# Optimization experiments

Measured on AMD Instinct MI355X. Metric: run time of the kernel, lower is better.

The kernel has to match this reference:

```python
import jax, jax.numpy as jnp
import numpy as np

S = 4  # MC samples


def _gat_layer(x, mask, w, a_src, a_dst, bias):
    # x: (b,n,fin)  w: (H,fin,fout)  mask: (b,n,n) bool
    h = jnp.einsum('bnf,hfo->bhno', x, w)                      # (b,H,n,fout)
    th = jnp.tanh(h)
    att_src = jnp.einsum('bhno,ho->bhn', th, a_src)
    att_dst = jnp.einsum('bhno,ho->bhn', th, a_dst)
    logits = jax.nn.leaky_relu(att_src[:, :, :, None] + att_dst[:, :, None, :], 0.2)
    logits = jnp.where(mask[:, None, :, :], logits, jnp.float32(-1e9))
    att = jax.nn.softmax(logits, axis=-1)                      # (b,H,n,n)
    out = jnp.einsum('bhij,bhjo->bhio', att, h) + bias         # (b,H,n,fout)
    return out, att


def setup_inputs() -> dict:
    key = jax.random.key(0)
    ks = jax.random.split(key, 11)
    b, n, f0, emb_d = 128, 128, 64, 64
    H1, f1, H2, f2 = 8, 16, 1, 2
    fin1 = f0 + emb_d            # 128 (n_units[0] += 64)
    fin2 = H1 * f1               # 128 (heads concatenated between layers)
    x = jax.random.normal(ks[0], (b, n, f0), jnp.float32)
    emb = jax.random.normal(ks[1], (b, n, emb_d), jnp.float32)
    adj = jax.random.randint(ks[2], (b, n, n), 0, 2).astype(jnp.int32)
    adj = jnp.maximum(adj, jnp.eye(n, dtype=jnp.int32)[None])  # self-loops keep softmax rows valid
    w1 = jax.random.normal(ks[3], (S, H1, fin1, f1), jnp.float32) * 0.1
    a_src1 = jax.random.normal(ks[4], (S, H1, f1), jnp.float32) * 0.1
    a_dst1 = jax.random.normal(ks[5], (S, H1, f1), jnp.float32) * 0.1
    b1 = jax.random.normal(ks[6], (f1,), jnp.float32) * 0.1
    w2 = jax.random.normal(ks[7], (S, H2, fin2, f2), jnp.float32) * 0.1
    a_src2 = jax.random.normal(ks[8], (S, H2, f2), jnp.float32) * 0.1
    a_dst2 = jax.random.normal(ks[9], (S, H2, f2), jnp.float32) * 0.1
    b2 = jax.random.normal(ks[10], (f2,), jnp.float32) * 0.1
    return dict(x=x, emb=emb, adj=adj, w1=w1, a_src1=a_src1, a_dst1=a_dst1, b1=b1,
                w2=w2, a_src2=a_src2, a_dst2=a_dst2, b2=b2)


def reference(x, emb, adj, w1, a_src1, a_dst1, b1, w2, a_src2, a_dst2, b2):
    mask = adj.astype(bool)
    x0 = jnp.concatenate([x, emb], axis=-1)                    # (b,n,128)
    b, n = x0.shape[0], x0.shape[1]
    xs = jnp.broadcast_to(x0, (S,) + x0.shape)                 # same input for each MC sample
    layer = jax.vmap(_gat_layer, in_axes=(0, None, 0, 0, 0, None))
    # layer 1 (per-sample variational weights), ELU activation
    h1, att1 = layer(xs, mask, w1, a_src1, a_dst1, b1)         # h1: (S,b,H1,n,f1)
    h1 = jax.nn.elu(h1)
    # concat heads: transpose(1,2).view(bs,n,-1)
    xs2 = jnp.transpose(h1, (0, 1, 3, 2, 4)).reshape(S, b, n, -1)
    # layer 2 (last layer): no activation, mean over heads
    h2, att2 = layer(xs2, mask, w2, a_src2, a_dst2, b2)        # (S,b,1,n,2)
    out = h2.mean(axis=2)                                      # (S,b,n,2)
    logp = jax.nn.log_softmax(out, axis=-1)[:, :, -1, :]       # (S,b,2) -> ego node
    result = jnp.mean(logp, axis=0)                            # var_mean -> mean (return_uncertainty=False)
    return result
```

## Files before the change

kernel.cpp:

```cpp
#include <hip/hip_runtime.h>
#include <stdint.h>
#include <math.h>

typedef __attribute__((ext_vector_type(8))) short short8;
typedef __attribute__((ext_vector_type(4))) float floatx4;

#define L_HF    0
#define L_SRC   16384
#define L_DST   18432
#define L_MASK  20480
#define L_H2P   22528
#define L_SIZE  26624

union F8 { short8 s8; uint32_t u[4]; };

#if __has_builtin(__builtin_amdgcn_exp2f)
#define EXP2F __builtin_amdgcn_exp2f
#else
#define EXP2F exp2f
#endif
#define LOG2E 1.4426950408889634f

__device__ __forceinline__ uint32_t packbf(float a, float b){
  uint32_t ua = __float_as_uint(a), ub = __float_as_uint(b);
  uint32_t ra = (ua + 0x7fffu + ((ua>>16)&1u)) >> 16;
  uint32_t rb = (ub + 0x7fffu + ((ub>>16)&1u)) >> 16;
  return ra | (rb<<16);
}
__device__ __forceinline__ uint32_t packbf_t(float a, float b){
  return __builtin_amdgcn_perm(__float_as_uint(b), __float_as_uint(a), 0x07060302u);
}
__device__ __forceinline__ float fast_tanh(float x){
  float e = __expf(2.f*x);
  return 1.f - 2.f*__builtin_amdgcn_rcpf(e + 1.f);
}

__global__ __launch_bounds__(512,8) void gat_fused(
    const float* __restrict__ x,  const float* __restrict__ emb,
    const int* __restrict__ adj,  const float* __restrict__ w1,
    const float* __restrict__ a_src1, const float* __restrict__ a_dst1,
    const float* __restrict__ b1, const float* __restrict__ w2,
    float* __restrict__ ws_h2)
{
  __shared__ __align__(16) char smem[L_SIZE];
  char*     hf    = smem + L_HF;
  uint32_t* hf_u  = (uint32_t*)(smem + L_HF);
  float*    src_l = (float*)(smem + L_SRC);
  float*    dst_l = (float*)(smem + L_DST);
  uint32_t* mask_l= (uint32_t*)(smem + L_MASK);
  const uint4* mask4 = (const uint4*)(smem + L_MASK);
  float2*   h2p   = (float2*)(smem + L_H2P);

  const int t    = threadIdx.x;
  const int blk  = blockIdx.x;
  const int s    = blk >> 8;
  const int bb   = (blk & 255) >> 1;
  const int half = blk & 1;
  const int lane = t & 63, w = t >> 6;
  const int of = lane & 15, kg = lane >> 4;

  const int arow = w*16 + of;
  const float* xrow = x   + ((size_t)bb*128 + arow)*64;
  const float* erow = emb + ((size_t)bb*128 + arow)*64;
  short8 af[4];
  #pragma unroll
  for (int ks=0; ks<4; ++ks){
    int k = ks*32 + kg*8;
    const float* p = (k<64) ? (xrow+k) : (erow + (k-64));
    float4 f0 = *(const float4*)p, f1 = *(const float4*)(p+4);
    F8 fr;
    fr.u[0]=packbf(f0.x,f0.y); fr.u[1]=packbf(f0.z,f0.w);
    fr.u[2]=packbf(f1.x,f1.y); fr.u[3]=packbf(f1.z,f1.w);
    af[ks]=fr.s8;
  }

  {
    const float* w1s = w1 + (size_t)s*16384 + half*8192;
    #pragma unroll
    for (int r=0; r<2; ++r){
      int q = t + r*512;
      int ql = q & 63, ks = (q>>6)&3, ct = q>>8;
      const float* wp = w1s + ct*2048 + (ks*32 + (ql>>4)*8)*16 + (ql&15);
      F8 fr;
      fr.u[0]=packbf(wp[0],  wp[16]);
      fr.u[1]=packbf(wp[32], wp[48]);
      fr.u[2]=packbf(wp[64], wp[80]);
      fr.u[3]=packbf(wp[96], wp[112]);
      *(short8*)(hf + ((ct*4+ks)*64 + ql)*16) = fr.s8;
    }
  }

  {
    const int* adjb = adj + (size_t)bb*16384;
    #pragma unroll 4
    for (int rr=0; rr<16; ++rr){
      const int row = w*16 + rr;
      const int* ar = adjb + row*128;
      uint64_t m0 = __ballot(ar[lane] != 0);
      uint64_t m1 = __ballot(ar[64+lane] != 0);
      if (lane == 0)
        ((uint4*)mask_l)[row] = make_uint4((uint32_t)m0,(uint32_t)(m0>>32),
                                           (uint32_t)m1,(uint32_t)(m1>>32));
    }
  }
  __syncthreads();

  floatx4 acc[4];
  #pragma unroll
  for (int ct=0; ct<4; ++ct) acc[ct]=(floatx4){0.f,0.f,0.f,0.f};
  #pragma unroll
  for (int ct=0; ct<4; ++ct)
    #pragma unroll
    for (int ks=0; ks<4; ++ks){
      short8 bfr = *(const short8*)(hf + ((ct*4+ks)*64 + lane)*16);
      acc[ct] = __builtin_amdgcn_mfma_f32_16x16x32_bf16(af[ks], bfr, acc[ct], 0,0,0);
    }
  __syncthreads();

  const int ks_h = w>>1, kgp = (w&1)*2 + (kg>>1), vv = (kg&1)*2;
  #pragma unroll
  for (int ct=0; ct<4; ++ct){
    const int ghd = half*4 + ct;
    float asv = a_src1[s*128 + ghd*16 + of] * LOG2E;
    float adv = a_dst1[s*128 + ghd*16 + of] * LOG2E;
    float ps[4], pd[4];
    #pragma unroll
    for (int r=0; r<4; ++r){
      float th = fast_tanh(acc[ct][r]);
      ps[r] = th*asv; pd[r] = th*adv;
    }
    #pragma unroll
    for (int off=1; off<16; off<<=1)
      #pragma unroll
      for (int r=0; r<4; ++r){ ps[r]+=__shfl_xor(ps[r],off); pd[r]+=__shfl_xor(pd[r],off); }
    if (of==0){
      #pragma unroll
      for (int r=0; r<4; ++r){
        int i = w*16 + kg*4 + r;
        src_l[ct*128+i]=ps[r]; dst_l[ct*128+i]=pd[r];
      }
    }
    uint32_t p0 = packbf(acc[ct][0], acc[ct][1]);
    uint32_t p1 = packbf(acc[ct][2], acc[ct][3]);
    uint32_t* dsth = hf_u + ((ct*4+ks_h)*64 + kgp*16 + of)*4 + vv;
    *(uint2*)dsth = make_uint2(p0, p1);
  }
  __syncthreads();

  const int lhd = w >> 1;
  const int ghd = half*4 + lhd;
  float b1v  = b1[of];
  float w2c0 = w2[s*256 + (ghd*16+of)*2 + 0];
  float w2c1 = w2[s*256 + (ghd*16+of)*2 + 1];
  short8 hb[4];
  #pragma unroll
  for (int ks=0; ks<4; ++ks)
    hb[ks] = *(const short8*)(hf + ((lhd*4+ks)*64 + lane)*16);

  #pragma unroll
  for (int rtl=0; rtl<4; ++rtl){
    const int rt = (w&1)*4 + rtl;
    const int im = rt*16 + of;
    float srcv = src_l[lhd*128 + im];
    uint4 mrow = mask4[im];
    floatx4 acc2 = (floatx4){0.f,0.f,0.f,0.f};
    float zp = 0.f;
    #pragma unroll
    for (int ks=0; ks<4; ++ks){
      const float* dp = dst_l + lhd*128 + ks*32 + kg*8;
      float4 d0 = *(const float4*)dp, d1 = *(const float4*)(dp+4);
      uint32_t mw = (ks==0)?mrow.x:(ks==1)?mrow.y:(ks==2)?mrow.z:mrow.w;
      uint32_t mbyte = mw >> (kg*8);
      float dj[8] = {d0.x,d0.y,d0.z,d0.w,d1.x,d1.y,d1.z,d1.w};
      float e[8];
      #pragma unroll
      for (int jj=0; jj<8; ++jj){
        float t0 = srcv + dj[jj];
        float lr = fmaxf(t0, 0.2f*t0);
        float ev = EXP2F(lr);
        ev = ((mbyte>>jj)&1u) ? ev : 0.f;
        e[jj]=ev; zp += ev;
      }
      F8 fr;
      fr.u[0]=packbf_t(e[0],e[1]); fr.u[1]=packbf_t(e[2],e[3]);
      fr.u[2]=packbf_t(e[4],e[5]); fr.u[3]=packbf_t(e[6],e[7]);
      acc2 = __builtin_amdgcn_mfma_f32_16x16x32_bf16(fr.s8, hb[ks], acc2, 0,0,0);
    }
    float zr = zp + __shfl_xor(zp,16); zr += __shfl_xor(zr,32);
    float zi = __builtin_amdgcn_rcpf(zr);
    float pc0[4], pc1[4];
    #pragma unroll
    for (int r=0; r<4; ++r){
      float ziR = __shfl(zi, kg*4+r);
      float o  = fmaf(acc2[r], ziR, b1v);
      float oe = (o>0.f) ? o : (__expf(o)-1.f);
      pc0[r]=oe*w2c0; pc1[r]=oe*w2c1;
    }
    #pragma unroll
    for (int off=1; off<16; off<<=1)
      #pragma unroll
      for (int r=0; r<4; ++r){ pc0[r]+=__shfl_xor(pc0[r],off); pc1[r]+=__shfl_xor(pc1[r],off); }
    if (of==0){
      #pragma unroll
      for (int r=0; r<4; ++r){
        int i = rt*16 + kg*4 + r;
        h2p[lhd*128 + i] = make_float2(pc0[r], pc1[r]);
      }
    }
  }
  __syncthreads();

  if (t < 256){
    const int jn = t>>1, cc = t&1;
    float hv = 0.f;
    #pragma unroll
    for (int hd2=0; hd2<4; ++hd2){
      float2 p = h2p[hd2*128+jn];
      hv += cc ? p.y : p.x;
    }
    ws_h2[(size_t)blk*256 + t] = hv;
  }
}

__global__ __launch_bounds__(256) void gat_tail(
    const float* __restrict__ ws_h2, const int* __restrict__ adj,
    const float* __restrict__ a_src2, const float* __restrict__ a_dst2,
    const float* __restrict__ b2, float* __restrict__ out)
{
  __shared__ float d2_l[128];
  __shared__ float red[16];
  __shared__ float srcE;
  const int bb = blockIdx.x, t = threadIdx.x;
  const int jn = t>>1, cc = t&1, lane = t&63, w = t>>6;
  const uint32_t bit = (adj[((size_t)bb*128+127)*128 + jn] != 0) ? 1u : 0u;
  float acc0=0.f, acc1=0.f;
  for (int s=0; s<4; ++s){
    float hv = ws_h2[(size_t)(s*256 + bb*2 + 0)*256 + t]
             + ws_h2[(size_t)(s*256 + bb*2 + 1)*256 + t];
    float th2 = fast_tanh(hv);
    float ps2 = th2*a_src2[s*2+cc];
    float pd2 = th2*a_dst2[s*2+cc];
    ps2 += __shfl_xor(ps2,1);
    pd2 += __shfl_xor(pd2,1);
    if (s) __syncthreads();
    if (cc==0) d2_l[jn]=pd2;
    if (t==254) srcE=ps2;
    __syncthreads();
    float t0 = srcE + d2_l[jn];
    float lg = fmaxf(t0, 0.2f*t0);
    float v  = bit ? lg : -1e9f;
    float mloc = v;
    #pragma unroll
    for (int off=32; off>=1; off>>=1) mloc = fmaxf(mloc, __shfl_xor(mloc,off));
    if (lane==0) red[w]=mloc;
    __syncthreads();
    float M = fmaxf(fmaxf(red[0],red[1]), fmaxf(red[2],red[3]));
    float e2 = __expf(v-M);
    float vA = e2*hv;
    float vZ = (cc==0) ? e2 : 0.f;
    #pragma unroll
    for (int off=2; off<=32; off<<=1){ vA+=__shfl_xor(vA,off); vZ+=__shfl_xor(vZ,off); }
    if (lane==0){ red[4+w]=vA; red[12+w]=vZ; }
    if (lane==1){ red[8+w]=vA; }
    __syncthreads();
    if (t==0){
      float S0 = red[4]+red[5]+red[6]+red[7];
      float S1 = red[8]+red[9]+red[10]+red[11];
      float Z  = red[12]+red[13]+red[14]+red[15];
      float o0 = S0/Z + b2[0];
      float o1 = S1/Z + b2[1];
      float mm = fmaxf(o0,o1);
      float lse = mm + logf(__expf(o0-mm)+__expf(o1-mm));
      acc0 += 0.25f*(o0 - lse);
      acc1 += 0.25f*(o1 - lse);
    }
  }
  if (t==0){ out[bb*2+0]=acc0; out[bb*2+1]=acc1; }
}

extern "C" void kernel_launch(void* const* d_in, const int* in_sizes, int n_in,
                              void* d_out, int out_size, void* d_ws, size_t ws_size,
                              hipStream_t stream) {
  const float* x      = (const float*)d_in[0];
  const float* emb    = (const float*)d_in[1];
  const int*   adj    = (const int*)d_in[2];
  const float* w1     = (const float*)d_in[3];
  const float* a_src1 = (const float*)d_in[4];
  const float* a_dst1 = (const float*)d_in[5];
  const float* b1     = (const float*)d_in[6];
  const float* w2     = (const float*)d_in[7];
  const float* a_src2 = (const float*)d_in[8];
  const float* a_dst2 = (const float*)d_in[9];
  const float* b2     = (const float*)d_in[10];

  float* ws_h2 = (float*)d_ws;

  gat_fused<<<dim3(1024), dim3(512), 0, stream>>>(x, emb, adj, w1, a_src1, a_dst1,
                                                  b1, w2, ws_h2);
  gat_tail<<<dim3(128), dim3(256), 0, stream>>>(ws_h2, adj, a_src2, a_dst2, b2,
                                                (float*)d_out);
}
```

Baseline: 139.0 us.

## Use DPP row reductions and interleave row tiles in attention-aggregation loop

```diff
diff --git a/kernel.cpp b/kernel.cpp
--- a/kernel.cpp
+++ b/kernel.cpp
@@ -33,6 +33,13 @@
 __device__ __forceinline__ float fast_tanh(float x){
   float e = __expf(2.f*x);
   return 1.f - 2.f*__builtin_amdgcn_rcpf(e + 1.f);
+}
+__device__ __forceinline__ float red16(float x){
+  x += __int_as_float(__builtin_amdgcn_update_dpp(0, __float_as_int(x), 0x128, 0xf, 0xf, true));
+  x += __int_as_float(__builtin_amdgcn_update_dpp(0, __float_as_int(x), 0x124, 0xf, 0xf, true));
+  x += __int_as_float(__builtin_amdgcn_update_dpp(0, __float_as_int(x), 0x122, 0xf, 0xf, true));
+  x += __int_as_float(__builtin_amdgcn_update_dpp(0, __float_as_int(x), 0x121, 0xf, 0xf, true));
+  return x;
 }
 
 __global__ __launch_bounds__(512,8) void gat_fused(
@@ -48,7 +55,6 @@
   float*    src_l = (float*)(smem + L_SRC);
   float*    dst_l = (float*)(smem + L_DST);
   uint32_t* mask_l= (uint32_t*)(smem + L_MASK);
-  const uint4* mask4 = (const uint4*)(smem + L_MASK);
   float2*   h2p   = (float2*)(smem + L_H2P);
 
   const int t    = threadIdx.x;
@@ -127,12 +133,8 @@
     #pragma unroll
     for (int r=0; r<4; ++r){
       float th = fast_tanh(acc[ct][r]);
-      ps[r] = th*asv; pd[r] = th*adv;
-    }
-    #pragma unroll
-    for (int off=1; off<16; off<<=1)
-      #pragma unroll
-      for (int r=0; r<4; ++r){ ps[r]+=__shfl_xor(ps[r],off); pd[r]+=__shfl_xor(pd[r],off); }
+      ps[r] = red16(th*asv); pd[r] = red16(th*adv);
+    }
     if (of==0){
       #pragma unroll
       for (int r=0; r<4; ++r){
@@ -149,61 +151,62 @@
 
   const int lhd = w >> 1;
   const int ghd = half*4 + lhd;
+  const int rtb = (w&1)*4;
   float b1v  = b1[of];
   float w2c0 = w2[s*256 + (ghd*16+of)*2 + 0];
   float w2c1 = w2[s*256 + (ghd*16+of)*2 + 1];
-  short8 hb[4];
-  #pragma unroll
-  for (int ks=0; ks<4; ++ks)
-    hb[ks] = *(const short8*)(hf + ((lhd*4+ks)*64 + lane)*16);
-
-  #pragma unroll
-  for (int rtl=0; rtl<4; ++rtl){
-    const int rt = (w&1)*4 + rtl;
-    const int im = rt*16 + of;
-    float srcv = src_l[lhd*128 + im];
-    uint4 mrow = mask4[im];
-    floatx4 acc2 = (floatx4){0.f,0.f,0.f,0.f};
-    float zp = 0.f;
-    #pragma unroll
-    for (int ks=0; ks<4; ++ks){
-      const float* dp = dst_l + lhd*128 + ks*32 + kg*8;
-      float4 d0 = *(const float4*)dp, d1 = *(const float4*)(dp+4);
-      uint32_t mw = (ks==0)?mrow.x:(ks==1)?mrow.y:(ks==2)?mrow.z:mrow.w;
-      uint32_t mbyte = mw >> (kg*8);
-      float dj[8] = {d0.x,d0.y,d0.z,d0.w,d1.x,d1.y,d1.z,d1.w};
+  float srcv[4];
+  #pragma unroll
+  for (int r=0; r<4; ++r) srcv[r] = src_l[lhd*128 + (rtb+r)*16 + of];
+
+  floatx4 acc2[4];
+  float zp[4];
+  #pragma unroll
+  for (int r=0; r<4; ++r){ acc2[r]=(floatx4){0.f,0.f,0.f,0.f}; zp[r]=0.f; }
+
+  #pragma unroll
+  for (int ks=0; ks<4; ++ks){
+    const float* dp = dst_l + lhd*128 + ks*32 + kg*8;
+    float4 d0 = *(const float4*)dp, d1 = *(const float4*)(dp+4);
+    float dj[8] = {d0.x,d0.y,d0.z,d0.w,d1.x,d1.y,d1.z,d1.w};
+    short8 hbk = *(const short8*)(hf + ((lhd*4+ks)*64 + lane)*16);
+    #pragma unroll
+    for (int rt=0; rt<4; ++rt){
+      const int im = (rtb+rt)*16 + of;
+      uint32_t mbyte = mask_l[im*4 + ks] >> (kg*8);
       float e[8];
       #pragma unroll
       for (int jj=0; jj<8; ++jj){
-        float t0 = srcv + dj[jj];
+        float t0 = srcv[rt] + dj[jj];
         float lr = fmaxf(t0, 0.2f*t0);
         float ev = EXP2F(lr);
         ev = ((mbyte>>jj)&1u) ? ev : 0.f;
-        e[jj]=ev; zp += ev;
+        e[jj]=ev; zp[rt] += ev;
       }
       F8 fr;
       fr.u[0]=packbf_t(e[0],e[1]); fr.u[1]=packbf_t(e[2],e[3]);
       fr.u[2]=packbf_t(e[4],e[5]); fr.u[3]=packbf_t(e[6],e[7]);
-      acc2 = __builtin_amdgcn_mfma_f32_16x16x32_bf16(fr.s8, hb[ks], acc2, 0,0,0);
-    }
-    float zr = zp + __shfl_xor(zp,16); zr += __shfl_xor(zr,32);
+      acc2[rt] = __builtin_amdgcn_mfma_f32_16x16x32_bf16(fr.s8, hbk, acc2[rt], 0,0,0);
+    }
+  }
+
+  #pragma unroll
+  for (int rt=0; rt<4; ++rt){
+    float zr = zp[rt] + __shfl_xor(zp[rt],16); zr += __shfl_xor(zr,32);
     float zi = __builtin_amdgcn_rcpf(zr);
     float pc0[4], pc1[4];
     #pragma unroll
     for (int r=0; r<4; ++r){
       float ziR = __shfl(zi, kg*4+r);
-      float o  = fmaf(acc2[r], ziR, b1v);
+      float o  = fmaf(acc2[rt][r], ziR, b1v);
       float oe = (o>0.f) ? o : (__expf(o)-1.f);
-      pc0[r]=oe*w2c0; pc1[r]=oe*w2c1;
-    }
-    #pragma unroll
-    for (int off=1; off<16; off<<=1)
-      #pragma unroll
-      for (int r=0; r<4; ++r){ pc0[r]+=__shfl_xor(pc0[r],off); pc1[r]+=__shfl_xor(pc1[r],off); }
+      pc0[r] = red16(oe*w2c0);
+      pc1[r] = red16(oe*w2c1);
+    }
     if (of==0){
       #pragma unroll
       for (int r=0; r<4; ++r){
-        int i = rt*16 + kg*4 + r;
+        int i = (rtb+rt)*16 + kg*4 + r;
         h2p[lhd*128 + i] = make_float2(pc0[r], pc1[r]);
       }
     }
```

New measurement: 175.3 us. +26.2%, slower.
